# Optimization experiments

Hardware: AMD Instinct MI355X
Metric: run time of the kernel (lower is better)

The kernel has to match this reference:

```python
import jax, jax.numpy as jnp
import numpy as np

N, E, FIN, H, C = 100000, 1600000, 128, 64, 40
EPS = 1e-5

def setup_inputs() -> dict:
    key = jax.random.key(0)
    ks = jax.random.split(key, 20)
    inp = {
        'x': jax.random.normal(ks[0], (N, FIN), jnp.float32),
        'edge_idx': jax.random.randint(ks[1], (2, E), 0, N, dtype=jnp.int64),
        'W1': jax.random.normal(ks[2], (FIN, H), jnp.float32) / np.sqrt(FIN),
        'b1': jnp.zeros((H,), jnp.float32),
        'g1': jnp.ones((H,), jnp.float32),
        'be1': jnp.zeros((H,), jnp.float32),
        'm1': jax.random.normal(ks[3], (H,), jnp.float32) * 0.1,
        'v1': jax.random.uniform(ks[4], (H,), jnp.float32) + 0.5,
        'W2': jax.random.normal(ks[5], (H, H), jnp.float32) / np.sqrt(H),
        'b2': jnp.zeros((H,), jnp.float32),
        'g2': jnp.ones((H,), jnp.float32),
        'be2': jnp.zeros((H,), jnp.float32),
        'm2': jax.random.normal(ks[6], (H,), jnp.float32) * 0.1,
        'v2': jax.random.uniform(ks[7], (H,), jnp.float32) + 0.5,
        'W3': jax.random.normal(ks[8], (H, C), jnp.float32) / np.sqrt(H),
        'b3': jnp.zeros((C,), jnp.float32),
    }
    return inp

def reference(x, edge_idx, W1, b1, g1, be1, m1, v1, W2, b2, g2, be2, m2, v2, W3, b3):
    n = x.shape[0]
    loop = jnp.arange(n, dtype=edge_idx.dtype)
    row = jnp.concatenate([edge_idx[0], loop])  # source nodes (+ self loops)
    col = jnp.concatenate([edge_idx[1], loop])  # target nodes (+ self loops)
    # symmetric gcn_norm: deg from unit edge weights aggregated at target
    deg = jax.ops.segment_sum(jnp.ones_like(row, dtype=x.dtype), col, num_segments=n)
    dinv = jnp.where(deg > 0, jax.lax.rsqrt(deg), 0.0)
    norm = dinv[row] * dinv[col]  # [E+N]

    def conv(h, W, b):
        hl = h @ W                            # dense transform first (PyG order)
        msg = hl[row] * norm[:, None]         # gather + edge scale
        agg = jax.ops.segment_sum(msg, col, num_segments=n)  # scatter-add
        return agg + b

    def bn(h, g, be, m, v):  # eval-mode BatchNorm1d (running stats)
        return g * (h - m) * jax.lax.rsqrt(v + EPS) + be

    h = jax.nn.relu(bn(conv(x, W1, b1), g1, be1, m1, v1))
    h = jax.nn.relu(bn(conv(h, W2, b2), g2, be2, m2, v2))
    return conv(h, W3, b3)
```

## Files before the change

### kernel.cpp

```cpp
#include <hip/hip_runtime.h>
#include <hip/hip_fp16.h>

#define EPSV 1e-5f
#define NB  256
#define CAP 8192
#define BIN_ITER 4

typedef short short8 __attribute__((ext_vector_type(8)));
typedef _Float16 half8 __attribute__((ext_vector_type(8)));
typedef float f32x4 __attribute__((ext_vector_type(4)));

__device__ inline unsigned h2u(__half2 h) { union { __half2 h; unsigned u; } c; c.h = h; return c.u; }
__device__ inline __half2 u2h(unsigned u) { union { unsigned u; __half2 h; } c; c.u = u; return c.h; }


template<int K, int F, int NT>
__device__ inline void wprep_one(const float* __restrict__ W,
                                 unsigned short* __restrict__ out, int tid) {
    const int lane = tid & 63;
    const int nt = (tid >> 6) % NT;
    const int ks = tid / (64 * NT);
    const int col = nt * 16 + (lane & 15);
    const int k0 = ks * 32 + (lane >> 4) * 8;
    half8 h8, l8;
#pragma unroll
    for (int e = 0; e < 8; ++e) {
        const float w = (col < F) ? W[(size_t)(k0 + e) * F + col] : 0.f;
        const _Float16 h = (_Float16)w;
        h8[e] = h;
        l8[e] = (_Float16)(w - (float)h);
    }
    half8* dst = (half8*)(out + (size_t)tid * 16);
    dst[0] = h8;
    dst[1] = l8;
}

__global__ __launch_bounds__(256) void k_prep(const float* __restrict__ W1,
                                              const float* __restrict__ W2,
                                              const float* __restrict__ W3,
                                              unsigned short* __restrict__ wf1,
                                              unsigned short* __restrict__ wf2,
                                              unsigned short* __restrict__ wf3,
                                              int* __restrict__ bcnt) {
    const int bid = blockIdx.x;
    if (bid == 8) {
        if (threadIdx.x < NB) bcnt[threadIdx.x] = 0;
        return;
    }
    const int tid = bid * 256 + threadIdx.x;
    if (tid < 1024) wprep_one<128, 64, 4>(W1, wf1, tid);
    else if (tid < 1536) wprep_one<64, 64, 4>(W2, wf2, tid - 1024);
    else if (tid < 1920) wprep_one<64, 40, 3>(W3, wf3, tid - 1536);
}


__global__ __launch_bounds__(1024) void k_bin(const int* __restrict__ row,
                                              const int* __restrict__ col,
                                              int* __restrict__ bcnt,
                                              unsigned* __restrict__ bkt,
                                              int E, int npb) {
    __shared__ int hist[NB];
    __shared__ int fill[NB];
    const int tid = threadIdx.x;
    const int e0 = blockIdx.x * (1024 * BIN_ITER);
    if (tid < NB) hist[tid] = 0;
    __syncthreads();
    unsigned ent[BIN_ITER];
    int bb[BIN_ITER];
#pragma unroll
    for (int j = 0; j < BIN_ITER; ++j) {
        const int i = e0 + j * 1024 + tid;
        bb[j] = -1;
        ent[j] = 0;
        if (i < E) {
            const int c = col[i], r = row[i];
            const int b = c / npb;
            bb[j] = b;
            ent[j] = ((unsigned)(c - b * npb) << 17) | (unsigned)r;
            atomicAdd(&hist[b], 1);
        }
    }
    __syncthreads();
    if (tid < NB)
        fill[tid] = hist[tid] ? atomicAdd(&bcnt[tid], hist[tid]) : 0;
    __syncthreads();
#pragma unroll
    for (int j = 0; j < BIN_ITER; ++j) {
        if (bb[j] >= 0) {
            const int pos = atomicAdd(&fill[bb[j]], 1);
            if (pos < CAP)
                bkt[(size_t)bb[j] * CAP + pos] = ent[j];
        }
    }
}


__global__ __launch_bounds__(NB) void k_bscan(const int* __restrict__ bcnt,
                                              int* __restrict__ bbase,
                                              int* __restrict__ rowptr, int E, int n) {
    __shared__ int s[NB];
    const int t = threadIdx.x;
    const int v = min(bcnt[t], CAP);
    s[t] = v;
    __syncthreads();
    for (int off = 1; off < NB; off <<= 1) {
        int u = (t >= off) ? s[t - off] : 0;
        __syncthreads();
        s[t] += u;
        __syncthreads();
    }
    bbase[t] = s[t] - v;
    if (t == 0) rowptr[n] = E;
}


__global__ __launch_bounds__(256) void k_place(const int* __restrict__ bcnt,
                                               const int* __restrict__ bbase,
                                               const unsigned* __restrict__ bkt,
                                               int* __restrict__ rowptr,
                                               float* __restrict__ dinv,
                                               int* __restrict__ srcidx,
                                               int n, int npb) {
    __shared__ int hist[512];
    __shared__ int pfx[512];
    __shared__ unsigned ent[CAP];
    const int b = blockIdx.x;
    const int tid = threadIdx.x;
    const int c0 = b * npb;
    const int nn = min(npb, n - c0);
    if (nn <= 0) return;
    const int bc = min(bcnt[b], CAP);
    const int base = bbase[b];
    for (int j = tid; j < nn; j += 256) hist[j] = 0;
    __syncthreads();
    for (int i = tid; i < bc; i += 256) {
        const unsigned e = bkt[(size_t)b * CAP + i];
        ent[i] = e;
        atomicAdd(&hist[e >> 17], 1);
    }
    __syncthreads();
    if (tid == 0) {
        int run = base;
        for (int j = 0; j < nn; ++j) { pfx[j] = run; run += hist[j]; }
    }
    __syncthreads();
    for (int j = tid; j < nn; j += 256) {
        rowptr[c0 + j] = pfx[j];
        dinv[c0 + j] = rsqrtf((float)(hist[j] + 1));
    }
    __syncthreads();
    for (int i = tid; i < bc; i += 256) {
        const unsigned e = ent[i];
        const int pos = atomicAdd(&pfx[e >> 17], 1);
        srcidx[pos] = (int)(e & 0x1FFFFu);
    }
}


template<int K, int NT>
__global__ __launch_bounds__(256) void gemm_f32in(const float* __restrict__ X,
                                                  const unsigned short* __restrict__ wfrag,
                                                  const float* __restrict__ dinv,
                                                  __half2* __restrict__ Y, int n) {
    const int lane = threadIdx.x & 63;
    const int wv = threadIdx.x >> 6;
    const int row0 = blockIdx.x * 64 + wv * 16;
    const int arow = row0 + (lane & 15);
    const bool aval = arow < n;

    f32x4 acc[NT];
#pragma unroll
    for (int t = 0; t < NT; ++t) acc[t] = (f32x4){0.f, 0.f, 0.f, 0.f};

#pragma unroll
    for (int ks = 0; ks < K / 32; ++ks) {
        float av[8];
        if (aval) {
            const float* ap = X + (size_t)arow * K + ks * 32 + (lane >> 4) * 8;
            const float4 p0 = *reinterpret_cast<const float4*>(ap);
            const float4 p1 = *reinterpret_cast<const float4*>(ap + 4);
            av[0] = p0.x; av[1] = p0.y; av[2] = p0.z; av[3] = p0.w;
            av[4] = p1.x; av[5] = p1.y; av[6] = p1.z; av[7] = p1.w;
        } else {
#pragma unroll
            for (int e = 0; e < 8; ++e) av[e] = 0.f;
        }
        half8 ah, al;
#pragma unroll
        for (int e = 0; e < 8; ++e) {
            const _Float16 h = (_Float16)av[e];
            ah[e] = h;
            al[e] = (_Float16)(av[e] - (float)h);
        }
#pragma unroll
        for (int t = 0; t < NT; ++t) {
            const half8* bp = (const half8*)(wfrag + (((size_t)ks * NT + t) * 64 + lane) * 16);
            const half8 bh = bp[0];
            const half8 bl = bp[1];
            acc[t] = __builtin_amdgcn_mfma_f32_16x16x32_f16(ah, bh, acc[t], 0, 0, 0);
            acc[t] = __builtin_amdgcn_mfma_f32_16x16x32_f16(al, bh, acc[t], 0, 0, 0);
            acc[t] = __builtin_amdgcn_mfma_f32_16x16x32_f16(ah, bl, acc[t], 0, 0, 0);
        }
    }

    const int col = lane & 15;
    const int rg = lane >> 4;
#pragma unroll
    for (int r = 0; r < 4; ++r) {
        const int orow = row0 + rg * 4 + r;
        const float di = (orow < n) ? dinv[orow] : 0.f;
#pragma unroll
        for (int t = 0; t < NT; ++t) {
            const float val = acc[t][r] * di;
            const float oth = __shfl_xor(val, 1);
            if (!(lane & 1))
                Y[(size_t)orow * (NT * 8) + t * 8 + (col >> 1)] = __floats2half2_rn(val, oth);
        }
    }
}


template<int K, int NT, int MODE>
__global__ __launch_bounds__(256) void gemm_f16in(const unsigned short* __restrict__ X,
                                                  const unsigned short* __restrict__ wfrag,
                                                  const float* __restrict__ dinv,
                                                  const float* __restrict__ bias,
                                                  void* __restrict__ Yv, int n) {
    const int lane = threadIdx.x & 63;
    const int wv = threadIdx.x >> 6;
    const int row0 = blockIdx.x * 64 + wv * 16;
    const int arow = row0 + (lane & 15);
    const bool aval = arow < n;

    f32x4 acc[NT];
#pragma unroll
    for (int t = 0; t < NT; ++t) acc[t] = (f32x4){0.f, 0.f, 0.f, 0.f};

#pragma unroll
    for (int ks = 0; ks < K / 32; ++ks) {
        half8 ah = {0, 0, 0, 0, 0, 0, 0, 0};
        if (aval)
            ah = *(const half8*)(X + (size_t)arow * K + ks * 32 + (lane >> 4) * 8);
#pragma unroll
        for (int t = 0; t < NT; ++t) {
            const half8* bp = (const half8*)(wfrag + (((size_t)ks * NT + t) * 64 + lane) * 16);
            const half8 bh = bp[0];
            const half8 bl = bp[1];
            acc[t] = __builtin_amdgcn_mfma_f32_16x16x32_f16(ah, bh, acc[t], 0, 0, 0);
            acc[t] = __builtin_amdgcn_mfma_f32_16x16x32_f16(ah, bl, acc[t], 0, 0, 0);
        }
    }

    const int col = lane & 15;
    const int rg = lane >> 4;
#pragma unroll
    for (int r = 0; r < 4; ++r) {
        const int orow = row0 + rg * 4 + r;
        if (MODE == 0) {
            const float di = (orow < n) ? dinv[orow] : 0.f;
            __half2* Y = (__half2*)Yv;
#pragma unroll
            for (int t = 0; t < NT; ++t) {
                const float val = acc[t][r] * di;
                const float oth = __shfl_xor(val, 1);
                if (!(lane & 1))
                    Y[(size_t)orow * (NT * 8) + t * 8 + (col >> 1)] = __floats2half2_rn(val, oth);
            }
        } else {
            float* Y = (float*)Yv;
#pragma unroll
            for (int t = 0; t < NT; ++t) {
                const int oc = t * 16 + col;
                if (orow < n && oc < 40)
                    Y[(size_t)orow * 40 + oc] = acc[t][r] + bias[oc];
            }
        }
    }
}


template<int MODE>
__global__ __launch_bounds__(256) void k_gather(const __half2* __restrict__ in,
                                                const int* __restrict__ rowptr,
                                                const int* __restrict__ srcidx,
                                                const float* __restrict__ dinv,
                                                const float* __restrict__ b,
                                                const float* __restrict__ g,
                                                const float* __restrict__ be,
                                                const float* __restrict__ m,
                                                const float* __restrict__ v,
                                                __half2* __restrict__ out, int n) {
    __shared__ unsigned offs[4][64];
    const int lane = threadIdx.x & 63;
    const int wslot = threadIdx.x >> 6;
    const int half = lane >> 5;
    const int p = lane & 31;
    const int node = blockIdx.x * 4 + wslot;

    if (node >= n) {
        if (!half) out[(size_t)node * 32 + p] = u2h(0u);
        return;
    }

    const int s = rowptr[node], e = rowptr[node + 1];
    const unsigned pconst = (unsigned)p * 4u;
    const char* inb = (const char*)in;
    __half2 acc0 = u2h(0u), acc1 = u2h(0u), acc2 = u2h(0u), acc3 = u2h(0u);

    for (int base = s; base < e; base += 64) {
        const int c = min(64, e - base);
        unsigned idx = (unsigned)n;
        if (base + lane < e) idx = (unsigned)srcidx[base + lane];
        offs[wslot][lane] = idx * 128u;
        for (int k8 = 0; k8 < 32; k8 += 8) {
            if (2 * k8 >= c) break;
            unsigned o[8], u[8];
#pragma unroll
            for (int j = 0; j < 8; ++j) o[j] = offs[wslot][2 * (k8 + j) + half];
#pragma unroll
            for (int j = 0; j < 8; ++j)
                u[j] = *(const unsigned*)(inb + (size_t)(o[j] + pconst));
            acc0 = __hadd2(acc0, u2h(u[0])); acc1 = __hadd2(acc1, u2h(u[1]));
            acc2 = __hadd2(acc2, u2h(u[2])); acc3 = __hadd2(acc3, u2h(u[3]));
            acc0 = __hadd2(acc0, u2h(u[4])); acc1 = __hadd2(acc1, u2h(u[5]));
            acc2 = __hadd2(acc2, u2h(u[6])); acc3 = __hadd2(acc3, u2h(u[7]));
        }
    }
    __half2 acc = __hadd2(__hadd2(acc0, acc1), __hadd2(acc2, acc3));
    acc = __hadd2(acc, u2h(__shfl_xor(h2u(acc), 32)));
    float2 af = __half22float2(acc);
    const float2 sf = __half22float2(in[(size_t)node * 32 + p]);
    float ax = af.x + sf.x, ay = af.y + sf.y;

    const float di = dinv[node];
    float ox, oy;
    if (MODE == 2) {
        ox = ax * di; oy = ay * di;
    } else {
        const float2 bb = ((const float2*)b)[p];
        const float2 gg = ((const float2*)g)[p];
        const float2 bee = ((const float2*)be)[p];
        const float2 mm = ((const float2*)m)[p];
        const float2 vv = ((const float2*)v)[p];
        const float sx = gg.x * rsqrtf(vv.x + EPSV);
        const float sy = gg.y * rsqrtf(vv.y + EPSV);
        ox = fmaxf((ax * di + bb.x - mm.x) * sx + bee.x, 0.f);
        oy = fmaxf((ay * di + bb.y - mm.y) * sy + bee.y, 0.f);
        if (MODE == 1) { ox *= di; oy *= di; }
    }
    if (!half) out[(size_t)node * 32 + p] = __floats2half2_rn(ox, oy);
}


extern "C" void kernel_launch(void* const* d_in, const int* in_sizes, int n_in,
                              void* d_out, int out_size, void* d_ws, size_t ws_size,
                              hipStream_t stream) {
    const float* x   = (const float*)d_in[0];
    const int*   ei  = (const int*)d_in[1];
    const float* W1  = (const float*)d_in[2];
    const float* b1  = (const float*)d_in[3];
    const float* g1  = (const float*)d_in[4];
    const float* be1 = (const float*)d_in[5];
    const float* m1  = (const float*)d_in[6];
    const float* v1  = (const float*)d_in[7];
    const float* W2  = (const float*)d_in[8];
    const float* b2  = (const float*)d_in[9];
    const float* g2  = (const float*)d_in[10];
    const float* be2 = (const float*)d_in[11];
    const float* m2  = (const float*)d_in[12];
    const float* v2  = (const float*)d_in[13];
    const float* W3  = (const float*)d_in[14];
    const float* b3  = (const float*)d_in[15];

    const int n = in_sizes[0] / 128;
    const int E = in_sizes[1] / 2;
    const int* row  = ei;
    const int* colv = ei + E;
    const int npb = (n + NB - 1) / NB;
    const int gblk = (n >> 6) + 1;
    const int npad = gblk * 64;

    char* base = (char*)d_ws;
    size_t off = 0;
    auto alloc = [&](size_t bytes) -> char* {
        char* p = base + off;
        off += (bytes + 255) & ~(size_t)255;
        return p;
    };
    int*      bcnt   = (int*)     alloc((size_t)NB * 4);
    int*      bbase  = (int*)     alloc((size_t)NB * 4);
    unsigned* bkt    = (unsigned*)alloc((size_t)NB * CAP * 4);
    int*      rowptr = (int*)     alloc((size_t)(n + 1) * 4);
    int*      srcidx = (int*)     alloc((size_t)E * 4);
    float*    dinv   = (float*)   alloc((size_t)n * 4);
    __half2*  hls1u  = (__half2*) alloc((size_t)npad * 32 * 4);
    __half2*  h1u    = (__half2*) alloc((size_t)npad * 32 * 4);
    __half2*  hls2u  = (__half2*) alloc((size_t)npad * 32 * 4);
    __half2*  h2lsu  = (__half2*) alloc((size_t)npad * 32 * 4);
    __half2*  agg3u  = (__half2*) alloc((size_t)npad * 32 * 4);
    unsigned short* wf1 = (unsigned short*)alloc((size_t)(128/32) * 4 * 64 * 32);
    unsigned short* wf2 = (unsigned short*)alloc((size_t)(64/32) * 4 * 64 * 32);
    unsigned short* wf3 = (unsigned short*)alloc((size_t)(64/32) * 3 * 64 * 32);
    float*    outp   = (float*)d_out;

    k_prep<<<9, 256, 0, stream>>>(W1, W2, W3, wf1, wf2, wf3, bcnt);

    const int binblk = (E + 1024 * BIN_ITER - 1) / (1024 * BIN_ITER);
    k_bin<<<binblk, 1024, 0, stream>>>(row, colv, bcnt, bkt, E, npb);
    k_bscan<<<1, NB, 0, stream>>>(bcnt, bbase, rowptr, E, n);
    k_place<<<NB, 256, 0, stream>>>(bcnt, bbase, bkt, rowptr, dinv, srcidx, n, npb);

    const int ablk = npad / 4;
    gemm_f32in<128, 4><<<gblk, 256, 0, stream>>>(x, wf1, dinv, hls1u, n);
    k_gather<0><<<ablk, 256, 0, stream>>>(hls1u, rowptr, srcidx, dinv,
                                          b1, g1, be1, m1, v1, h1u, n);
    gemm_f16in<64, 4, 0><<<gblk, 256, 0, stream>>>((const unsigned short*)h1u, wf2,
                                                   dinv, nullptr, hls2u, n);
    k_gather<1><<<ablk, 256, 0, stream>>>(hls2u, rowptr, srcidx, dinv,
                                          b2, g2, be2, m2, v2, h2lsu, n);
    k_gather<2><<<ablk, 256, 0, stream>>>(h2lsu, rowptr, srcidx, dinv,
                                          nullptr, nullptr, nullptr, nullptr, nullptr,
                                          agg3u, n);
    gemm_f16in<64, 3, 1><<<gblk, 256, 0, stream>>>((const unsigned short*)agg3u, wf3,
                                                   dinv, b3, outp, n);
}
```

Before: 197.1 us.

## Use finer CSR buckets and persistent grid-stride gather waves

Raises the bucket count from 256 to 1024 and lowers per-bucket capacity from 8192 to 2048. This gives k_place four times as many blocks, each with smaller shared-memory histograms. The three gather kernels become grid-stride loops over a fixed 2048-block grid, with the BatchNorm parameter loads and rsqrt hoisted out of the per-node loop. The aim is more parallelism in CSR construction and less per-block setup in aggregation. The risks are overflowing the smaller bucket capacity on skewed graphs and weaker load balance with the persistent waves.

Measured after the change: 173.9 us, median of 3. -11.8%, faster.

```diff
diff --git a/kernel.cpp b/kernel.cpp
--- a/kernel.cpp
+++ b/kernel.cpp
@@ -2,8 +2,8 @@
 #include <hip/hip_fp16.h>
 
 #define EPSV 1e-5f
-#define NB  256
-#define CAP 8192
+#define NB  1024
+#define CAP 2048
 #define BIN_ITER 4
 
 typedef short short8 __attribute__((ext_vector_type(8)));
@@ -44,7 +44,7 @@
                                               int* __restrict__ bcnt) {
     const int bid = blockIdx.x;
     if (bid == 8) {
-        if (threadIdx.x < NB) bcnt[threadIdx.x] = 0;
+        for (int i = threadIdx.x; i < NB; i += 256) bcnt[i] = 0;
         return;
     }
     const int tid = bid * 256 + threadIdx.x;
@@ -121,8 +121,8 @@
                                                float* __restrict__ dinv,
                                                int* __restrict__ srcidx,
                                                int n, int npb) {
-    __shared__ int hist[512];
-    __shared__ int pfx[512];
+    __shared__ int hist[128];
+    __shared__ int pfx[128];
     __shared__ unsigned ent[CAP];
     const int b = blockIdx.x;
     const int tid = threadIdx.x;
@@ -289,66 +289,74 @@
                                                 const float* __restrict__ be,
                                                 const float* __restrict__ m,
                                                 const float* __restrict__ v,
-                                                __half2* __restrict__ out, int n) {
+                                                __half2* __restrict__ out,
+                                                int n, int npad) {
     __shared__ unsigned offs[4][64];
     const int lane = threadIdx.x & 63;
     const int wslot = threadIdx.x >> 6;
     const int half = lane >> 5;
     const int p = lane & 31;
-    const int node = blockIdx.x * 4 + wslot;
-
-    if (node >= n) {
-        if (!half) out[(size_t)node * 32 + p] = u2h(0u);
-        return;
-    }
-
-    const int s = rowptr[node], e = rowptr[node + 1];
+    const int wid0 = blockIdx.x * 4 + wslot;
+    const int nwaves = gridDim.x * 4;
     const unsigned pconst = (unsigned)p * 4u;
     const char* inb = (const char*)in;
-    __half2 acc0 = u2h(0u), acc1 = u2h(0u), acc2 = u2h(0u), acc3 = u2h(0u);
-
-    for (int base = s; base < e; base += 64) {
-        const int c = min(64, e - base);
-        unsigned idx = (unsigned)n;
-        if (base + lane < e) idx = (unsigned)srcidx[base + lane];
-        offs[wslot][lane] = idx * 128u;
-        for (int k8 = 0; k8 < 32; k8 += 8) {
-            if (2 * k8 >= c) break;
-            unsigned o[8], u[8];
-#pragma unroll
-            for (int j = 0; j < 8; ++j) o[j] = offs[wslot][2 * (k8 + j) + half];
-#pragma unroll
-            for (int j = 0; j < 8; ++j)
-                u[j] = *(const unsigned*)(inb + (size_t)(o[j] + pconst));
-            acc0 = __hadd2(acc0, u2h(u[0])); acc1 = __hadd2(acc1, u2h(u[1]));
-            acc2 = __hadd2(acc2, u2h(u[2])); acc3 = __hadd2(acc3, u2h(u[3]));
-            acc0 = __hadd2(acc0, u2h(u[4])); acc1 = __hadd2(acc1, u2h(u[5]));
-            acc2 = __hadd2(acc2, u2h(u[6])); acc3 = __hadd2(acc3, u2h(u[7]));
-        }
-    }
-    __half2 acc = __hadd2(__hadd2(acc0, acc1), __hadd2(acc2, acc3));
-    acc = __hadd2(acc, u2h(__shfl_xor(h2u(acc), 32)));
-    float2 af = __half22float2(acc);
-    const float2 sf = __half22float2(in[(size_t)node * 32 + p]);
-    float ax = af.x + sf.x, ay = af.y + sf.y;
-
-    const float di = dinv[node];
-    float ox, oy;
-    if (MODE == 2) {
-        ox = ax * di; oy = ay * di;
-    } else {
-        const float2 bb = ((const float2*)b)[p];
+
+    float sx = 0.f, sy = 0.f;
+    float2 bb = {0.f, 0.f}, mm = {0.f, 0.f}, bee = {0.f, 0.f};
+    if (MODE != 2) {
+        bb = ((const float2*)b)[p];
         const float2 gg = ((const float2*)g)[p];
-        const float2 bee = ((const float2*)be)[p];
-        const float2 mm = ((const float2*)m)[p];
+        bee = ((const float2*)be)[p];
+        mm = ((const float2*)m)[p];
         const float2 vv = ((const float2*)v)[p];
-        const float sx = gg.x * rsqrtf(vv.x + EPSV);
-        const float sy = gg.y * rsqrtf(vv.y + EPSV);
-        ox = fmaxf((ax * di + bb.x - mm.x) * sx + bee.x, 0.f);
-        oy = fmaxf((ay * di + bb.y - mm.y) * sy + bee.y, 0.f);
-        if (MODE == 1) { ox *= di; oy *= di; }
-    }
-    if (!half) out[(size_t)node * 32 + p] = __floats2half2_rn(ox, oy);
+        sx = gg.x * rsqrtf(vv.x + EPSV);
+        sy = gg.y * rsqrtf(vv.y + EPSV);
+    }
+
+    for (int node = wid0; node < npad; node += nwaves) {
+        if (node >= n) {
+            if (!half) out[(size_t)node * 32 + p] = u2h(0u);
+            continue;
+        }
+        const int s = rowptr[node], e = rowptr[node + 1];
+        __half2 acc0 = u2h(0u), acc1 = u2h(0u), acc2 = u2h(0u), acc3 = u2h(0u);
+
+        for (int base = s; base < e; base += 64) {
+            const int c = min(64, e - base);
+            unsigned idx = (unsigned)n;
+            if (base + lane < e) idx = (unsigned)srcidx[base + lane];
+            offs[wslot][lane] = idx * 128u;
+            for (int k8 = 0; k8 < 32; k8 += 8) {
+                if (2 * k8 >= c) break;
+                unsigned o[8], u[8];
+#pragma unroll
+                for (int j = 0; j < 8; ++j) o[j] = offs[wslot][2 * (k8 + j) + half];
+#pragma unroll
+                for (int j = 0; j < 8; ++j)
+                    u[j] = *(const unsigned*)(inb + (size_t)(o[j] + pconst));
+                acc0 = __hadd2(acc0, u2h(u[0])); acc1 = __hadd2(acc1, u2h(u[1]));
+                acc2 = __hadd2(acc2, u2h(u[2])); acc3 = __hadd2(acc3, u2h(u[3]));
+                acc0 = __hadd2(acc0, u2h(u[4])); acc1 = __hadd2(acc1, u2h(u[5]));
+                acc2 = __hadd2(acc2, u2h(u[6])); acc3 = __hadd2(acc3, u2h(u[7]));
+            }
+        }
+        __half2 acc = __hadd2(__hadd2(acc0, acc1), __hadd2(acc2, acc3));
+        acc = __hadd2(acc, u2h(__shfl_xor(h2u(acc), 32)));
+        float2 af = __half22float2(acc);
+        const float2 sf = __half22float2(in[(size_t)node * 32 + p]);
+        const float ax = af.x + sf.x, ay = af.y + sf.y;
+
+        const float di = dinv[node];
+        float ox, oy;
+        if (MODE == 2) {
+            ox = ax * di; oy = ay * di;
+        } else {
+            ox = fmaxf((ax * di + bb.x - mm.x) * sx + bee.x, 0.f);
+            oy = fmaxf((ay * di + bb.y - mm.y) * sy + bee.y, 0.f);
+            if (MODE == 1) { ox *= di; oy *= di; }
+        }
+        if (!half) out[(size_t)node * 32 + p] = __floats2half2_rn(ox, oy);
+    }
 }
 
 
@@ -410,17 +418,17 @@
     k_bscan<<<1, NB, 0, stream>>>(bcnt, bbase, rowptr, E, n);
     k_place<<<NB, 256, 0, stream>>>(bcnt, bbase, bkt, rowptr, dinv, srcidx, n, npb);
 
-    const int ablk = npad / 4;
+    const int ablk = 2048;
     gemm_f32in<128, 4><<<gblk, 256, 0, stream>>>(x, wf1, dinv, hls1u, n);
     k_gather<0><<<ablk, 256, 0, stream>>>(hls1u, rowptr, srcidx, dinv,
-                                          b1, g1, be1, m1, v1, h1u, n);
+                                          b1, g1, be1, m1, v1, h1u, n, npad);
     gemm_f16in<64, 4, 0><<<gblk, 256, 0, stream>>>((const unsigned short*)h1u, wf2,
                                                    dinv, nullptr, hls2u, n);
     k_gather<1><<<ablk, 256, 0, stream>>>(hls2u, rowptr, srcidx, dinv,
-                                          b2, g2, be2, m2, v2, h2lsu, n);
+                                          b2, g2, be2, m2, v2, h2lsu, n, npad);
     k_gather<2><<<ablk, 256, 0, stream>>>(h2lsu, rowptr, srcidx, dinv,
                                           nullptr, nullptr, nullptr, nullptr, nullptr,
-                                          agg3u, n);
+                                          agg3u, n, npad);
     gemm_f16in<64, 3, 1><<<gblk, 256, 0, stream>>>((const unsigned short*)agg3u, wf3,
                                                    dinv, b3, outp, n);
 }
```
